# Kernel tuning notes

Measured on AMD Instinct MI355X. Metric: run time of the kernel, lower is better.

## Reference

```python
import jax, jax.numpy as jnp
import numpy as np

SOW_INIT = 1e-10  # sum_of_weights_initial_value
EPS = 1e-8       # torch.nn.CosineSimilarity default eps


def setup_inputs() -> dict:
    key = jax.random.key(0)
    k1, k2, k3 = jax.random.split(key, 3)
    input_image = jax.random.normal(k1, (1, 3, 224, 224), dtype=jnp.float32)
    masks = jax.random.uniform(k2, (1000, 224, 224), dtype=jnp.float32)
    # Linear encoder: flattened image [3*224*224] -> feature dim 128
    W = jax.random.normal(k3, (3, 224, 224, 128), dtype=jnp.float32) * 0.01
    return {"input_image": input_image, "masks": masks, "W": W}


def reference(input_image, masks, W):
    img = input_image[0]  # [3, H, W]
    # Encoder applied to (img * mask): rep_n = sum_chw (img*mask)[c,h,w] * W[c,h,w,f]
    # Precompute A[h,w,f] = sum_c img[c,h,w] * W[c,h,w,f] so masked reps never
    # materialize the [N,3,H,W] masked-image tensor.
    A = jnp.einsum('chw,chwf->hwf', img, W)          # [H, W, F]
    rep0 = jnp.sum(A, axis=(0, 1))                   # unmasked representation [F]
    reps = jnp.einsum('nhw,hwf->nf', masks, A)       # masked representations [N, F]

    # Cosine similarity (dim=1), clamped norms as in torch
    n0 = jnp.maximum(jnp.linalg.norm(rep0), EPS)
    nr = jnp.maximum(jnp.linalg.norm(reps, axis=1), EPS)
    sims = (reps @ rep0) / (nr * n0)                 # [N]

    H, Wd = masks.shape[1], masks.shape[2]
    imp0 = jnp.zeros((H, Wd), dtype=jnp.float32)
    unc0 = jnp.zeros((H, Wd), dtype=jnp.float32)
    sow0 = jnp.full((H, Wd), SOW_INIT, dtype=jnp.float32)

    def step(carry, inp):
        imp, unc, sow = carry
        m, s = inp  # mask [H,W], similarity scalar
        sow = sow + m
        prev = imp
        imp = imp + m * (s - imp) / sow
        unc = unc + (s - imp) * (s - prev) * m
        return (imp, unc, sow), None

    (imp, unc, sow), _ = jax.lax.scan(step, (imp0, unc0, sow0), (masks, sims))
    return jnp.stack([imp, unc, sow])  # [3, H, W]
```

## Files before the change

### kernel.cpp

```cpp
#include <hip/hip_runtime.h>
#include <hip/hip_bf16.h>
#include <stdint.h>

#define HWN 50176
#define NM  1000
#define FD  128
#define NSPLIT 49
#define KSTEPS 32
#define NSCAN 20
#define NPB 50

typedef __attribute__((ext_vector_type(8))) short short8;
typedef __attribute__((ext_vector_type(4))) float f32x4;

__device__ __forceinline__ unsigned short f2bf(float x) {
    union { float f; unsigned u; } v; v.f = x;
    unsigned r = v.u + 0x7FFFu + ((v.u >> 16) & 1u);
    return (unsigned short)(r >> 16);
}

#define AS1(p) ((const __attribute__((address_space(1))) unsigned int*)(p))
#define AS3(p) ((__attribute__((address_space(3))) unsigned int*)(p))

__global__ __launch_bounds__(256) void k_encode(const float* __restrict__ img,
                                                const float* __restrict__ Wt,
                                                unsigned short* __restrict__ Bpack,
                                                float* __restrict__ rep0part)
{
    const int t = threadIdx.x;
    const int f = t & 127;
    const int kt = blockIdx.x * 2 + (t >> 7);
    const int hw0 = kt * 32;
    float vals[32];
    float rsum = 0.f;
#pragma unroll
    for (int e = 0; e < 32; ++e) {
        const int hw = hw0 + e;
        float a = img[hw] * Wt[(size_t)hw * FD + f];
        a = fmaf(img[HWN + hw],     Wt[(size_t)(HWN + hw) * FD + f], a);
        a = fmaf(img[2 * HWN + hw], Wt[(size_t)(2 * HWN + hw) * FD + f], a);
        vals[e] = a;
        rsum += a;
    }
    char* tile = (char*)Bpack + (size_t)kt * 8192 + f * 64;
#pragma unroll
    for (int j = 0; j < 4; ++j) {
        short8 pk;
#pragma unroll
        for (int e = 0; e < 8; ++e) pk[e] = (short)f2bf(vals[j * 8 + e]);
        *reinterpret_cast<short8*>(tile + ((j ^ (f & 3)) << 4)) = pk;
    }
    __shared__ float red[256];
    red[t] = rsum;
    __syncthreads();
    if (t < 128) rep0part[(size_t)blockIdx.x * 128 + f] = red[t] + red[t + 128];
}

__global__ __launch_bounds__(256) void k_rep0red(const float* __restrict__ rep0part,
                                                 float* __restrict__ rep0)
{
    const int f = blockIdx.x;
    float s = 0.f;
    for (int b = threadIdx.x; b < 784; b += 256) s += rep0part[(size_t)b * 128 + f];
    __shared__ float red[256];
    red[threadIdx.x] = s;
    __syncthreads();
    for (int o = 128; o > 0; o >>= 1) {
        if (threadIdx.x < o) red[threadIdx.x] += red[threadIdx.x + o];
        __syncthreads();
    }
    if (threadIdx.x == 0) rep0[f] = red[0];
}

__global__ __launch_bounds__(256, 4) void k_gemm(const float* __restrict__ masks,
                                                 const unsigned short* __restrict__ Bpack,
                                                 float* __restrict__ partial)
{
    __shared__ __align__(16) unsigned short Bs[2][4096];

    const int t = threadIdx.x;
    const int wv = t >> 6, lane = t & 63;
    const int lrow = lane & 15, lslot = lane >> 4;
    const int mtile = blockIdx.x, split = blockIdx.y;

    int row = mtile * 64 + wv * 16 + lrow;
    if (row >= NM) row = NM - 1;
    const float* aptr = masks + (size_t)row * HWN + split * 1024 + lslot * 8;
    const char* bsrc = (const char*)Bpack + (size_t)(split * KSTEPS) * 8192 + t * 16;
    char* dst0 = (char*)&Bs[0][0] + t * 16;
    char* dst1 = (char*)&Bs[1][0] + t * 16;
    const int rdoff = lrow * 64 + ((lslot ^ (lrow & 3)) << 4);

    f32x4 acc[8];
#pragma unroll
    for (int i = 0; i < 8; ++i) acc[i] = f32x4{0.f, 0.f, 0.f, 0.f};

    __builtin_amdgcn_global_load_lds(AS1(bsrc), AS3(dst0), 16, 0, 0);
    __builtin_amdgcn_global_load_lds(AS1(bsrc + 4096), AS3(dst0 + 4096), 16, 0, 0);
    f32x4 a0 = *reinterpret_cast<const f32x4*>(aptr);
    f32x4 a1 = *reinterpret_cast<const f32x4*>(aptr + 4);

    for (int ks = 0; ks < KSTEPS; ++ks) {
        const int cur = ks & 1;
        __syncthreads();
        if (ks + 1 < KSTEPS) {
            char* nd = cur ? dst0 : dst1;
            const char* nsrc = bsrc + (size_t)(ks + 1) * 8192;
            __builtin_amdgcn_global_load_lds(AS1(nsrc), AS3(nd), 16, 0, 0);
            __builtin_amdgcn_global_load_lds(AS1(nsrc + 4096), AS3(nd + 4096), 16, 0, 0);
        }
        const int kn = (ks + 1 < KSTEPS) ? (ks + 1) : ks;
        f32x4 na0 = *reinterpret_cast<const f32x4*>(aptr + kn * 32);
        f32x4 na1 = *reinterpret_cast<const f32x4*>(aptr + kn * 32 + 4);

        union { short8 s; __hip_bfloat162 h[4]; } apk;
        apk.h[0] = __float22bfloat162_rn(float2{a0[0], a0[1]});
        apk.h[1] = __float22bfloat162_rn(float2{a0[2], a0[3]});
        apk.h[2] = __float22bfloat162_rn(float2{a1[0], a1[1]});
        apk.h[3] = __float22bfloat162_rn(float2{a1[2], a1[3]});

        const char* bbase = (const char*)&Bs[cur][0] + rdoff;
#pragma unroll
        for (int ft = 0; ft < 8; ++ft) {
            short8 bfv = *reinterpret_cast<const short8*>(bbase + ft * 1024);
            acc[ft] = __builtin_amdgcn_mfma_f32_16x16x32_bf16(apk.s, bfv, acc[ft], 0, 0, 0);
        }
        a0 = na0; a1 = na1;
    }

    const int crow = mtile * 64 + wv * 16 + (lslot << 2);
    float* pb = partial + ((size_t)split * 1024 + crow) * FD + lrow;
#pragma unroll
    for (int ft = 0; ft < 8; ++ft)
#pragma unroll
        for (int r = 0; r < 4; ++r)
            __builtin_nontemporal_store(acc[ft][r], pb + (size_t)r * FD + ft * 16);
}

__global__ __launch_bounds__(128) void k_sims(const float* __restrict__ partial,
                                              const float* __restrict__ rep0,
                                              float* __restrict__ sims)
{
    const int n = blockIdx.x;
    const int f = threadIdx.x;
    float r = 0.f;
    for (int s = 0; s < NSPLIT; ++s)
        r += __builtin_nontemporal_load(partial + ((size_t)s * 1024 + n) * FD + f);
    const float r0 = rep0[f];
    __shared__ float red0[128], red1[128], red2[128];
    red0[f] = r * r0;
    red1[f] = r * r;
    red2[f] = r0 * r0;
    __syncthreads();
    for (int o = 64; o > 0; o >>= 1) {
        if (f < o) {
            red0[f] += red0[f + o];
            red1[f] += red1[f + o];
            red2[f] += red2[f + o];
        }
        __syncthreads();
    }
    if (f == 0) {
        const float nr = fmaxf(sqrtf(red1[0]), 1e-8f);
        const float nz = fmaxf(sqrtf(red2[0]), 1e-8f);
        sims[n] = red0[0] / (nr * nz);
    }
}

__global__ __launch_bounds__(256) void k_colsums(const float* __restrict__ masks,
                                                 const float* __restrict__ sims,
                                                 float* __restrict__ Spart)
{
    __shared__ float s1v[NPB], s2v[NPB];
    const int t = threadIdx.x;
    const int split = blockIdx.y;
    if (t < NPB) {
        const float s = sims[split * NPB + t];
        s1v[t] = s;
        s2v[t] = s * s;
    }
    __syncthreads();
    const int pix = (blockIdx.x * 256 + t) * 4;
    const float* mp = masks + (size_t)split * NPB * HWN + pix;
    f32x4 s0 = {0.f,0.f,0.f,0.f}, s1 = s0, s2 = s0;
#pragma unroll 5
    for (int i = 0; i < NPB; ++i) {
        const f32x4 m = *reinterpret_cast<const f32x4*>(mp + (size_t)i * HWN);
        const float a = s1v[i], b = s2v[i];
        s0 += m;
#pragma unroll
        for (int e = 0; e < 4; ++e) {
            s1[e] = fmaf(m[e], a, s1[e]);
            s2[e] = fmaf(m[e], b, s2[e]);
        }
    }
    float* sp = Spart + (size_t)split * 3 * HWN + pix;
    __builtin_nontemporal_store(s0, reinterpret_cast<f32x4*>(sp));
    __builtin_nontemporal_store(s1, reinterpret_cast<f32x4*>(sp + HWN));
    __builtin_nontemporal_store(s2, reinterpret_cast<f32x4*>(sp + 2 * HWN));
}

__global__ __launch_bounds__(256) void k_final(const float* __restrict__ Spart,
                                               float* __restrict__ out)
{
    const int pix = (blockIdx.x * 256 + threadIdx.x) * 4;
    f32x4 s0 = {0.f,0.f,0.f,0.f}, s1 = s0, s2 = s0;
#pragma unroll 4
    for (int sp = 0; sp < NSCAN; ++sp) {
        const float* p = Spart + (size_t)sp * 3 * HWN + pix;
        s0 += __builtin_nontemporal_load(reinterpret_cast<const f32x4*>(p));
        s1 += __builtin_nontemporal_load(reinterpret_cast<const f32x4*>(p + HWN));
        s2 += __builtin_nontemporal_load(reinterpret_cast<const f32x4*>(p + 2 * HWN));
    }
    f32x4 imp, unc, sow;
#pragma unroll
    for (int e = 0; e < 4; ++e) {
        sow[e] = 1e-10f + s0[e];
        imp[e] = s1[e] / sow[e];
        unc[e] = fmaf(-imp[e], s1[e], s2[e]);
    }
    *reinterpret_cast<f32x4*>(out + pix) = imp;
    *reinterpret_cast<f32x4*>(out + HWN + pix) = unc;
    *reinterpret_cast<f32x4*>(out + 2 * HWN + pix) = sow;
}

extern "C" void kernel_launch(void* const* d_in, const int* in_sizes, int n_in,
                              void* d_out, int out_size, void* d_ws, size_t ws_size,
                              hipStream_t stream) {
    const float* img   = (const float*)d_in[0];
    const float* masks = (const float*)d_in[1];
    const float* Wt    = (const float*)d_in[2];
    float* out = (float*)d_out;

    char* ws = (char*)d_ws;
    unsigned short* Bpack = (unsigned short*)ws;
    float* partial  = (float*)(ws + 12845056);
    float* rep0part = partial;
    float* rep0     = (float*)(ws + 38535168);
    float* sims     = (float*)(ws + 38535680);
    float* Spart    = (float*)ws;

    hipLaunchKernelGGL(k_encode,  dim3(784), dim3(256), 0, stream, img, Wt, Bpack, rep0part);
    hipLaunchKernelGGL(k_rep0red, dim3(128), dim3(256), 0, stream, rep0part, rep0);
    hipLaunchKernelGGL(k_gemm,    dim3(16, NSPLIT), dim3(256), 0, stream, masks, Bpack, partial);
    hipLaunchKernelGGL(k_sims,    dim3(NM), dim3(128), 0, stream, partial, rep0, sims);
    hipLaunchKernelGGL(k_colsums, dim3(49, NSCAN), dim3(256), 0, stream, masks, sims, Spart);
    hipLaunchKernelGGL(k_final,   dim3(49), dim3(256), 0, stream, Spart, out);
}
```

Measured before the change: 148.5 us.

## Stage mask tiles through LDS with triple-buffered async loads in GEMM

The GEMM kernel now loads both the fp32 mask tile and the bf16 encoder tile into LDS through global_load_lds, using a three-stage ring buffer with explicit vmcnt waits and barriers. Before, each thread loaded masks straight into registers one step ahead. The B tile layout written by the encoder is changed to a rotated-row swizzle to match the new LDS read pattern, and MFMA issue is bracketed with raised priority. The goal is deeper prefetch that hides memory latency, at the cost of more LDS per block (48KB), which lowers occupancy to 3 blocks per CU.

After: 131.1 us. -11.7%, faster.

```diff
diff --git a/kernel.cpp b/kernel.cpp
--- a/kernel.cpp
+++ b/kernel.cpp
@@ -42,13 +42,13 @@
         vals[e] = a;
         rsum += a;
     }
-    char* tile = (char*)Bpack + (size_t)kt * 8192 + f * 64;
+    char* tile = (char*)Bpack + (size_t)kt * 8192;
 #pragma unroll
     for (int j = 0; j < 4; ++j) {
         short8 pk;
 #pragma unroll
         for (int e = 0; e < 8; ++e) pk[e] = (short)f2bf(vals[j * 8 + e]);
-        *reinterpret_cast<short8*>(tile + ((j ^ (f & 3)) << 4)) = pk;
+        *reinterpret_cast<short8*>(tile + j * 2048 + (((f + j) & 127) << 4)) = pk;
     }
     __shared__ float red[256];
     red[t] = rsum;
@@ -72,69 +72,98 @@
     if (threadIdx.x == 0) rep0[f] = red[0];
 }
 
-__global__ __launch_bounds__(256, 4) void k_gemm(const float* __restrict__ masks,
+__global__ __launch_bounds__(256, 3) void k_gemm(const float* __restrict__ masks,
                                                  const unsigned short* __restrict__ Bpack,
                                                  float* __restrict__ partial)
 {
-    __shared__ __align__(16) unsigned short Bs[2][4096];
+    __shared__ __align__(16) char lds[3][16384];
 
     const int t = threadIdx.x;
     const int wv = t >> 6, lane = t & 63;
-    const int lrow = lane & 15, lslot = lane >> 4;
+    const int lrow = lane & 15, kg = lane >> 4;
     const int mtile = blockIdx.x, split = blockIdx.y;
-
-    int row = mtile * 64 + wv * 16 + lrow;
-    if (row >= NM) row = NM - 1;
-    const float* aptr = masks + (size_t)row * HWN + split * 1024 + lslot * 8;
-    const char* bsrc = (const char*)Bpack + (size_t)(split * KSTEPS) * 8192 + t * 16;
-    char* dst0 = (char*)&Bs[0][0] + t * 16;
-    char* dst1 = (char*)&Bs[1][0] + t * 16;
-    const int rdoff = lrow * 64 + ((lslot ^ (lrow & 3)) << 4);
+    const int n0 = mtile * 64;
+
+    const int s1 = 256 + t;
+    const int ar0 = t >> 3, ar1 = s1 >> 3;
+    const int ac0 = (t & 7) ^ (ar0 & 7);
+    const int ac1 = (t & 7) ^ (ar1 & 7);
+    int arow0 = n0 + ar0; if (arow0 >= NM) arow0 = NM - 1;
+    int arow1 = n0 + ar1; if (arow1 >= NM) arow1 = NM - 1;
+    const float* aSrc0 = masks + (size_t)arow0 * HWN + split * 1024 + ac0 * 4;
+    const float* aSrc1 = masks + (size_t)arow1 * HWN + split * 1024 + ac1 * 4;
+    const char*  bSrc  = (const char*)Bpack + (size_t)split * KSTEPS * 8192 + t * 16;
+
+    const int r = wv * 16 + lrow;
+    const int ao0 = r * 128 + (((2 * kg)     ^ (r & 7)) << 4);
+    const int ao1 = r * 128 + ((((2 * kg)+1) ^ (r & 7)) << 4);
+    int bo[8];
+#pragma unroll
+    for (int ft = 0; ft < 8; ++ft)
+        bo[ft] = 8192 + kg * 2048 + (((ft * 16 + lrow + kg) & 127) << 4);
 
     f32x4 acc[8];
 #pragma unroll
     for (int i = 0; i < 8; ++i) acc[i] = f32x4{0.f, 0.f, 0.f, 0.f};
 
-    __builtin_amdgcn_global_load_lds(AS1(bsrc), AS3(dst0), 16, 0, 0);
-    __builtin_amdgcn_global_load_lds(AS1(bsrc + 4096), AS3(dst0 + 4096), 16, 0, 0);
-    f32x4 a0 = *reinterpret_cast<const f32x4*>(aptr);
-    f32x4 a1 = *reinterpret_cast<const f32x4*>(aptr + 4);
-
+#define STAGE(KS, BUF) do {                                                             \
+        char* base_ = &lds[BUF][0];                                                     \
+        __builtin_amdgcn_global_load_lds(AS1(aSrc0 + (KS) * 32), AS3(base_ + t * 16), 16, 0, 0);          \
+        __builtin_amdgcn_global_load_lds(AS1(aSrc1 + (KS) * 32), AS3(base_ + 4096 + t * 16), 16, 0, 0);   \
+        __builtin_amdgcn_global_load_lds(AS1(bSrc + (size_t)(KS) * 8192),        AS3(base_ + 8192 + t * 16), 16, 0, 0);        \
+        __builtin_amdgcn_global_load_lds(AS1(bSrc + (size_t)(KS) * 8192 + 4096), AS3(base_ + 12288 + t * 16), 16, 0, 0);       \
+    } while (0)
+
+    STAGE(0, 0);
+    STAGE(1, 1);
+    asm volatile("s_waitcnt vmcnt(4)" ::: "memory");
+    __builtin_amdgcn_s_barrier();
+    __builtin_amdgcn_sched_barrier(0);
+
+    int cur = 0, stg = 2;
     for (int ks = 0; ks < KSTEPS; ++ks) {
-        const int cur = ks & 1;
-        __syncthreads();
-        if (ks + 1 < KSTEPS) {
-            char* nd = cur ? dst0 : dst1;
-            const char* nsrc = bsrc + (size_t)(ks + 1) * 8192;
-            __builtin_amdgcn_global_load_lds(AS1(nsrc), AS3(nd), 16, 0, 0);
-            __builtin_amdgcn_global_load_lds(AS1(nsrc + 4096), AS3(nd + 4096), 16, 0, 0);
+        if (ks + 2 < KSTEPS) STAGE(ks + 2, stg);
+
+        const char* A = &lds[cur][0];
+        const f32x4 alo = *reinterpret_cast<const f32x4*>(A + ao0);
+        const f32x4 ahi = *reinterpret_cast<const f32x4*>(A + ao1);
+        union { short8 s; __hip_bfloat162 h[4]; } apk;
+        apk.h[0] = __float22bfloat162_rn(float2{alo[0], alo[1]});
+        apk.h[1] = __float22bfloat162_rn(float2{alo[2], alo[3]});
+        apk.h[2] = __float22bfloat162_rn(float2{ahi[0], ahi[1]});
+        apk.h[3] = __float22bfloat162_rn(float2{ahi[2], ahi[3]});
+        short8 bfv[8];
+#pragma unroll
+        for (int ft = 0; ft < 8; ++ft)
+            bfv[ft] = *reinterpret_cast<const short8*>(A + bo[ft]);
+
+        asm volatile("s_waitcnt lgkmcnt(0)" ::: "memory");
+        __builtin_amdgcn_sched_barrier(0);
+        __builtin_amdgcn_s_setprio(1);
+#pragma unroll
+        for (int ft = 0; ft < 8; ++ft)
+            acc[ft] = __builtin_amdgcn_mfma_f32_16x16x32_bf16(apk.s, bfv[ft], acc[ft], 0, 0, 0);
+        __builtin_amdgcn_s_setprio(0);
+        __builtin_amdgcn_sched_barrier(0);
+
+        if (ks < KSTEPS - 2)       asm volatile("s_waitcnt vmcnt(4)" ::: "memory");
+        else if (ks == KSTEPS - 2) asm volatile("s_waitcnt vmcnt(0)" ::: "memory");
+        if (ks < KSTEPS - 1) {
+            __builtin_amdgcn_s_barrier();
+            __builtin_amdgcn_sched_barrier(0);
         }
-        const int kn = (ks + 1 < KSTEPS) ? (ks + 1) : ks;
-        f32x4 na0 = *reinterpret_cast<const f32x4*>(aptr + kn * 32);
-        f32x4 na1 = *reinterpret_cast<const f32x4*>(aptr + kn * 32 + 4);
-
-        union { short8 s; __hip_bfloat162 h[4]; } apk;
-        apk.h[0] = __float22bfloat162_rn(float2{a0[0], a0[1]});
-        apk.h[1] = __float22bfloat162_rn(float2{a0[2], a0[3]});
-        apk.h[2] = __float22bfloat162_rn(float2{a1[0], a1[1]});
-        apk.h[3] = __float22bfloat162_rn(float2{a1[2], a1[3]});
-
-        const char* bbase = (const char*)&Bs[cur][0] + rdoff;
-#pragma unroll
-        for (int ft = 0; ft < 8; ++ft) {
-            short8 bfv = *reinterpret_cast<const short8*>(bbase + ft * 1024);
-            acc[ft] = __builtin_amdgcn_mfma_f32_16x16x32_bf16(apk.s, bfv, acc[ft], 0, 0, 0);
-        }
-        a0 = na0; a1 = na1;
-    }
-
-    const int crow = mtile * 64 + wv * 16 + (lslot << 2);
+        cur = (cur + 1 == 3) ? 0 : cur + 1;
+        stg = (stg + 1 == 3) ? 0 : stg + 1;
+    }
+#undef STAGE
+
+    const int crow = n0 + wv * 16 + (kg << 2);
     float* pb = partial + ((size_t)split * 1024 + crow) * FD + lrow;
 #pragma unroll
     for (int ft = 0; ft < 8; ++ft)
 #pragma unroll
-        for (int r = 0; r < 4; ++r)
-            __builtin_nontemporal_store(acc[ft][r], pb + (size_t)r * FD + ft * 16);
+        for (int rr = 0; rr < 4; ++rr)
+            __builtin_nontemporal_store(acc[ft][rr], pb + (size_t)rr * FD + ft * 16);
 }
 
 __global__ __launch_bounds__(128) void k_sims(const float* __restrict__ partial,
@@ -143,13 +172,13 @@
 {
     const int n = blockIdx.x;
     const int f = threadIdx.x;
-    float r = 0.f;
+    float rsum = 0.f;
     for (int s = 0; s < NSPLIT; ++s)
-        r += __builtin_nontemporal_load(partial + ((size_t)s * 1024 + n) * FD + f);
+        rsum += __builtin_nontemporal_load(partial + ((size_t)s * 1024 + n) * FD + f);
     const float r0 = rep0[f];
     __shared__ float red0[128], red1[128], red2[128];
-    red0[f] = r * r0;
-    red1[f] = r * r;
+    red0[f] = rsum * r0;
+    red1[f] = rsum * rsum;
     red2[f] = r0 * r0;
     __syncthreads();
     for (int o = 64; o > 0; o >>= 1) {
```
